# Optimization experiments

Measured on AMD Instinct MI355X. Metric: run time of the kernel, lower is better.

## Reference

```python
import jax, jax.numpy as jnp
import numpy as np

N_TOKENS = 65536
D_MODEL = 256
N_EXPERTS = 32
NEG_INF = -1e38


def setup_inputs() -> dict:
    key = jax.random.key(0)
    k_x, k_wg, k_wn, k_we, k_noise = jax.random.split(key, 5)
    x = jax.random.normal(k_x, (N_TOKENS, D_MODEL), dtype=jnp.float32)
    # gating and noise projections: Linear(d_model -> n_experts), no bias
    Wg = jax.random.normal(k_wg, (D_MODEL, N_EXPERTS), dtype=jnp.float32) * 0.02
    Wnoise = jax.random.normal(k_wn, (D_MODEL, N_EXPERTS), dtype=jnp.float32) * 0.02
    # experts: one Linear(d_model -> d_model) per expert
    We = jax.random.normal(k_we, (N_EXPERTS, D_MODEL, D_MODEL), dtype=jnp.float32) * 0.02
    be = jnp.zeros((N_EXPERTS, D_MODEL), dtype=jnp.float32)
    # torch.randn(nexperts): one shared noise vector broadcast over tokens
    noise_vec = jax.random.normal(k_noise, (N_EXPERTS,), dtype=jnp.float32)
    return {"x": x, "Wg": Wg, "Wnoise": Wnoise, "We": We, "be": be,
            "noise_vec": noise_vec, "top_k": 2}


def reference(x, Wg, Wnoise, We, be, noise_vec, top_k):
    # Eq. (4): H = x Wg + randn * softplus(x Wnoise)   -> [N, E]
    g = x @ Wg
    H = g + noise_vec[None, :] * jax.nn.softplus(x @ Wnoise)
    # Keep top_k largest per row (original masks the bottom E-k with -Inf)
    vals, idx = jax.lax.top_k(H, top_k)                      # [N, k]
    rows = jnp.arange(H.shape[0])[:, None]
    keep = jnp.full_like(H, NEG_INF).at[rows, idx].set(vals)  # [N, E]
    G = jax.nn.softmax(keep, axis=1)                          # [N, E], k nonzeros
    # Dense all-expert compute (as in the original): E_out [N, E, D]
    E_out = jnp.einsum('nd,edh->neh', x, We) + be[None, :, :]
    # Weighted sum over experts
    return jnp.einsum('ne,neh->nh', G, E_out)                 # [N, D]
```

## Files before the change

### kernel.cpp

```cpp
#include <hip/hip_runtime.h>

#define NT 65536
#define DM 256
#define NE 32

typedef __attribute__((ext_vector_type(8))) short v8bf;
typedef __attribute__((ext_vector_type(4))) float v4f;

#define C_RISKY 0
#define C_TC1 1
#define C_TC2 2
#define C_HIST1 8
#define C_HIST2 40
#define C_CUR1 72
#define C_CUR2 104

__device__ __forceinline__ unsigned short f2bf(float f) {
  union { float f; unsigned u; } v; v.f = f;
  unsigned r = v.u + 0x7FFFu + ((v.u >> 16) & 1u);
  return (unsigned short)(r >> 16);
}

#define GLOAD_LDS16(g, l)                                                     \
  __builtin_amdgcn_global_load_lds(                                           \
      (const __attribute__((address_space(1))) unsigned int*)(g),             \
      (__attribute__((address_space(3))) unsigned int*)(l), 16, 0, 0)

__global__ __launch_bounds__(256) void convert_kernel(const float* __restrict__ x,
                                                      unsigned short* __restrict__ xbf) {
  size_t i = (size_t)blockIdx.x * 256 + threadIdx.x;
  const float4* s = (const float4*)x + i * 2;
  float4 a = s[0], b = s[1];
  union { v8bf v; unsigned short u[8]; uint4 q; } p;
  p.u[0] = f2bf(a.x); p.u[1] = f2bf(a.y); p.u[2] = f2bf(a.z); p.u[3] = f2bf(a.w);
  p.u[4] = f2bf(b.x); p.u[5] = f2bf(b.y); p.u[6] = f2bf(b.z); p.u[7] = f2bf(b.w);
  *(uint4*)(xbf + i * 8) = p.q;
}

__global__ __launch_bounds__(256) void prep_w(const float* __restrict__ Wg,
                                              const float* __restrict__ Wn,
                                              float* __restrict__ wgn,
                                              unsigned short* __restrict__ wgnb) {
  int i = blockIdx.x * 256 + threadIdx.x;
  if (i < 256 * 64) {
    int k = i >> 6, c = i & 63;
    float v = (c < 32) ? Wg[k * 32 + c] : Wn[k * 32 + (c - 32)];
    wgn[i] = v;
    wgnb[c * 256 + k] = f2bf(v);
  }
}

__global__ __launch_bounds__(256) void prep_wet(const float* __restrict__ We,
                                                unsigned short* __restrict__ WeT) {
  __shared__ float t[32][33];
  int e = blockIdx.x;
  int d0 = (blockIdx.y >> 3) * 32, h0 = (blockIdx.y & 7) * 32;
  int tx = threadIdx.x & 31, ty = threadIdx.x >> 5;
  const float* src = We + ((size_t)e * 256 + d0) * 256 + h0;
#pragma unroll
  for (int r = 0; r < 4; ++r) t[ty + r * 8][tx] = src[(size_t)(ty + r * 8) * 256 + tx];
  __syncthreads();
  unsigned short* dst = WeT + ((size_t)e * 256 + h0) * 256 + d0;
#pragma unroll
  for (int r = 0; r < 4; ++r) dst[(size_t)(ty + r * 8) * 256 + tx] = f2bf(t[tx][ty + r * 8]);
}

__global__ __launch_bounds__(256) void gate_kernel(const float* __restrict__ x,
                                                   const unsigned short* __restrict__ xbf,
                                                   int use_xbf,
                                                   const unsigned short* __restrict__ wgnb,
                                                   const float* __restrict__ nvec,
                                                   int4* __restrict__ records,
                                                   int* __restrict__ risky,
                                                   int* __restrict__ ctrl) {
  __shared__ __align__(16) union {
    struct { short Al[128 * 64]; short Bl[64 * 64]; } t;
    float H[128 * 67];
  } sm;
  __shared__ float nvs[32];
  __shared__ int lh[64];
  int tid = threadIdx.x;
  if (tid < 64) lh[tid] = 0;
  if (tid < 32) nvs[tid] = nvec[tid];
  int t0 = blockIdx.x * 128;
  int lane = tid & 63, wid = tid >> 6;
  int wm = wid * 32;
  int lm = lane & 15, lk8 = (lane >> 4) * 8;
  int r0 = tid >> 3, kc = tid & 7;
  int kcs = kc ^ (r0 & 7);
  v4f acc[2][4];
  v4f zero = {0.f, 0.f, 0.f, 0.f};
#pragma unroll
  for (int mi = 0; mi < 2; ++mi)
#pragma unroll
    for (int ni = 0; ni < 4; ++ni) acc[mi][ni] = zero;
  for (int k0 = 0; k0 < 256; k0 += 64) {
    __syncthreads();
    if (use_xbf) {
#pragma unroll
      for (int j = 0; j < 4; ++j)
        GLOAD_LDS16(xbf + ((size_t)(t0 + r0 + 32 * j) * 256 + k0 + kcs * 8),
                    sm.t.Al + (size_t)(256 * j + (tid & 192)) * 8);
#pragma unroll
      for (int j = 0; j < 2; ++j)
        GLOAD_LDS16(wgnb + ((size_t)(r0 + 32 * j) * 256 + k0 + kcs * 8),
                    sm.t.Bl + (size_t)(256 * j + (tid & 192)) * 8);
    } else {
#pragma unroll
      for (int j = 0; j < 4; ++j) {
        const float4* s = (const float4*)(x + ((size_t)(t0 + r0 + 32 * j) * 256 + k0 + kcs * 8));
        float4 a = s[0], b = s[1];
        union { v8bf v; unsigned short u[8]; } p;
        p.u[0] = f2bf(a.x); p.u[1] = f2bf(a.y); p.u[2] = f2bf(a.z); p.u[3] = f2bf(a.w);
        p.u[4] = f2bf(b.x); p.u[5] = f2bf(b.y); p.u[6] = f2bf(b.z); p.u[7] = f2bf(b.w);
        *(v8bf*)(sm.t.Al + (size_t)(tid + 256 * j) * 8) = p.v;
      }
#pragma unroll
      for (int j = 0; j < 2; ++j) {
        uint4 w = *(const uint4*)(wgnb + ((size_t)(r0 + 32 * j) * 256 + k0 + kcs * 8));
        *(uint4*)(sm.t.Bl + (size_t)(tid + 256 * j) * 8) = w;
      }
    }
    __syncthreads();
#pragma unroll
    for (int ks = 0; ks < 64; ks += 32) {
      int c = (ks + lk8) >> 3;
      int cs = c ^ (lm & 7);
      v8bf af[2], bfr[4];
#pragma unroll
      for (int mi = 0; mi < 2; ++mi) {
        int r = wm + mi * 16 + lm;
        af[mi] = *(const v8bf*)(sm.t.Al + (size_t)(r * 8 + cs) * 8);
      }
#pragma unroll
      for (int ni = 0; ni < 4; ++ni) {
        int cr = ni * 16 + lm;
        bfr[ni] = *(const v8bf*)(sm.t.Bl + (size_t)(cr * 8 + cs) * 8);
      }
#pragma unroll
      for (int mi = 0; mi < 2; ++mi)
#pragma unroll
        for (int ni = 0; ni < 4; ++ni)
          acc[mi][ni] = __builtin_amdgcn_mfma_f32_16x16x32_bf16(af[mi], bfr[ni], acc[mi][ni], 0, 0, 0);
    }
  }
  __syncthreads();
  int cg = lane & 15, rg = lane >> 4;
#pragma unroll
  for (int mi = 0; mi < 2; ++mi)
#pragma unroll
    for (int r = 0; r < 4; ++r) {
      int row = wm + mi * 16 + rg * 4 + r;
#pragma unroll
      for (int ni = 0; ni < 4; ++ni) sm.H[row * 67 + ni * 16 + cg] = acc[mi][ni][r];
    }
  __syncthreads();
  if (tid < 128) {
    int t = t0 + tid;
    float v1 = -3e38f, v2 = -3e38f, v3 = -3e38f;
    int i1 = 0, i2 = 0;
#pragma unroll 4
    for (int e = 0; e < 32; ++e) {
      float g = sm.H[tid * 67 + e];
      float n = sm.H[tid * 67 + 32 + e];
      float sp = fmaxf(n, 0.f) + log1pf(expf(-fabsf(n)));
      float he = fmaf(nvs[e], sp, g);
      if (he > v1) { v3 = v2; v2 = v1; i2 = i1; v1 = he; i1 = e; }
      else if (he > v2) { v3 = v2; v2 = he; i2 = e; }
      else if (he > v3) v3 = he;
    }
    float w1v = 1.f / (1.f + expf(v2 - v1));
    float w2v = 1.f / (1.f + expf(v1 - v2));
    records[t] = make_int4(i1, i2, __float_as_int(w1v), __float_as_int(w2v));
    atomicAdd(&lh[i1], 1);
    atomicAdd(&lh[32 + i2], 1);
    if (v2 - v3 < 2e-2f) {
      int p = atomicAdd(&ctrl[C_RISKY], 1);
      risky[p] = t;
    }
  }
  __syncthreads();
  if (tid < 32) atomicAdd(&ctrl[C_HIST1 + tid], lh[tid]);
  else if (tid < 64) atomicAdd(&ctrl[C_HIST2 + (tid - 32)], lh[tid]);
}

__global__ __launch_bounds__(256) void fixup_kernel(const float* __restrict__ x,
                                                    const float* __restrict__ wgn,
                                                    const float* __restrict__ nvec,
                                                    int4* __restrict__ records,
                                                    const int* __restrict__ risky,
                                                    int* __restrict__ ctrl) {
  int cnt = ctrl[C_RISKY];
  int lane = threadIdx.x & 63, wid = threadIdx.x >> 6;
  for (int r = blockIdx.x * 4 + wid; r < cnt; r += gridDim.x * 4) {
    int t = __builtin_amdgcn_readfirstlane(risky[r]);
    const float* xr = x + (size_t)t * 256;
    double a0 = 0.0, a1 = 0.0, a2 = 0.0, a3 = 0.0;
    for (int k = 0; k < 256; k += 4) {
      float4 xv = *(const float4*)(xr + k);
      a0 = fma((double)xv.x, (double)wgn[(k + 0) * 64 + lane], a0);
      a1 = fma((double)xv.y, (double)wgn[(k + 1) * 64 + lane], a1);
      a2 = fma((double)xv.z, (double)wgn[(k + 2) * 64 + lane], a2);
      a3 = fma((double)xv.w, (double)wgn[(k + 3) * 64 + lane], a3);
    }
    double acc = (a0 + a1) + (a2 + a3);
    double sv = __shfl(acc, lane + 32);
    double H;
    if (lane < 32) {
      double sp = fmax(sv, 0.0) + log1p(exp(-fabs(sv)));
      H = acc + (double)nvec[lane] * sp;
    } else
      H = -1e300;
    double v = H; int idx = lane;
#pragma unroll
    for (int off = 32; off >= 1; off >>= 1) {
      double ov = __shfl_xor(v, off); int oi = __shfl_xor(idx, off);
      if (ov > v || (ov == v && oi < idx)) { v = ov; idx = oi; }
    }
    int i1 = idx; double v1 = v;
    v = (lane == i1) ? -1e300 : H; idx = lane;
#pragma unroll
    for (int off = 32; off >= 1; off >>= 1) {
      double ov = __shfl_xor(v, off); int oi = __shfl_xor(idx, off);
      if (ov > v || (ov == v && oi < idx)) { v = ov; idx = oi; }
    }
    int i2 = idx; double v2 = v;
    if (lane == 0) {
      float w1v = (float)(1.0 / (1.0 + exp(v2 - v1)));
      float w2v = (float)(1.0 / (1.0 + exp(v1 - v2)));
      int4 old = records[t];
      if (old.x != i1) { atomicSub(&ctrl[C_HIST1 + old.x], 1); atomicAdd(&ctrl[C_HIST1 + i1], 1); }
      if (old.y != i2) { atomicSub(&ctrl[C_HIST2 + old.y], 1); atomicAdd(&ctrl[C_HIST2 + i2], 1); }
      records[t] = make_int4(i1, i2, __float_as_int(w1v), __float_as_int(w2v));
    }
  }
}

__global__ __launch_bounds__(64) void scan_kernel(int* __restrict__ ctrl,
                                                  int4* __restrict__ table1,
                                                  int4* __restrict__ table2) {
  __shared__ int so1[32], so2[32], tp1[32], tp2[32];
  int tid = threadIdx.x;
  if (tid == 0) {
    int o = 0, tp = 0;
    for (int e = 0; e < 32; ++e) {
      so1[e] = o; tp1[e] = tp;
      int c = ctrl[C_HIST1 + e];
      o += c; tp += (c + 127) >> 7;
    }
    ctrl[C_TC1] = tp;
    o = 0; tp = 0;
    for (int e = 0; e < 32; ++e) {
      so2[e] = o; tp2[e] = tp;
      int c = ctrl[C_HIST2 + e];
      o += c; tp += (c + 127) >> 7;
    }
    ctrl[C_TC2] = tp;
  }
  __syncthreads();
  if (tid < 32) {
    int e = tid;
    ctrl[C_CUR1 + e] = so1[e];
    int c = ctrl[C_HIST1 + e];
    int nt = (c + 127) >> 7;
    for (int m = 0; m < nt; ++m)
      table1[tp1[e] + m] = make_int4(e, so1[e] + m * 128, min(128, c - m * 128), 0);
  } else if (tid < 64) {
    int e = tid - 32;
    ctrl[C_CUR2 + e] = so2[e];
    int c = ctrl[C_HIST2 + e];
    int nt = (c + 127) >> 7;
    for (int m = 0; m < nt; ++m)
      table2[tp2[e] + m] = make_int4(e, so2[e] + m * 128, min(128, c - m * 128), 0);
  }
}

__global__ __launch_bounds__(256) void scatter_kernel(const int4* __restrict__ records,
                                                      int* __restrict__ ctrl,
                                                      int* __restrict__ perm1, float* __restrict__ pw1,
                                                      int* __restrict__ perm2, float* __restrict__ pw2) {
  __shared__ int lh1[32], lh2[32], b1[32], b2[32];
  int tid = threadIdx.x;
  if (tid < 32) { lh1[tid] = 0; lh2[tid] = 0; }
  __syncthreads();
  int t = blockIdx.x * 256 + tid;
  int4 rec = records[t];
  int r1 = atomicAdd(&lh1[rec.x], 1);
  int r2 = atomicAdd(&lh2[rec.y], 1);
  __syncthreads();
  if (tid < 32) {
    b1[tid] = atomicAdd(&ctrl[C_CUR1 + tid], lh1[tid]);
    b2[tid] = atomicAdd(&ctrl[C_CUR2 + tid], lh2[tid]);
  }
  __syncthreads();
  int s1 = b1[rec.x] + r1; perm1[s1] = t; pw1[s1] = __int_as_float(rec.z);
  int s2 = b2[rec.y] + r2; perm2[s2] = t; pw2[s2] = __int_as_float(rec.w);
}

__global__ __launch_bounds__(256) void expert_kernel(const float* __restrict__ x,
                                                     const unsigned short* __restrict__ xbf,
                                                     int use_xbf,
                                                     const unsigned short* __restrict__ WeT,
                                                     const float* __restrict__ be,
                                                     const int* __restrict__ perm,
                                                     const float* __restrict__ pw,
                                                     const int4* __restrict__ table,
                                                     const int* __restrict__ tcp,
                                                     float* __restrict__ out,
                                                     int accumulate) {
  int nt = *tcp;
  if (blockIdx.x >= nt) return;
  int4 ent = table[blockIdx.x];
  int e = ent.x, sbase = ent.y, rows = ent.z;
  int n0 = blockIdx.y * 128;
  __shared__ __align__(16) short Al[128 * 64];
  __shared__ __align__(16) short Bl[128 * 64];
  int tid = threadIdx.x;
  int lane = tid & 63, wid = tid >> 6;
  int wm = (wid & 1) * 64, wn = (wid >> 1) * 64;
  int lm = lane & 15, lk8 = (lane >> 4) * 8;
  int r0 = tid >> 3, kc = tid & 7;
  int kcs = kc ^ (r0 & 7);
  int tok[4];
#pragma unroll
  for (int j = 0; j < 4; ++j) tok[j] = perm[sbase + min(r0 + 32 * j, rows - 1)];
  v4f acc[4][4];
  v4f zero = {0.f, 0.f, 0.f, 0.f};
#pragma unroll
  for (int mi = 0; mi < 4; ++mi)
#pragma unroll
    for (int ni = 0; ni < 4; ++ni) acc[mi][ni] = zero;
  for (int k0 = 0; k0 < 256; k0 += 64) {
    __syncthreads();
    if (use_xbf) {
#pragma unroll
      for (int j = 0; j < 4; ++j)
        GLOAD_LDS16(xbf + ((size_t)tok[j] * 256 + k0 + kcs * 8),
                    Al + (size_t)(256 * j + (tid & 192)) * 8);
#pragma unroll
      for (int j = 0; j < 4; ++j)
        GLOAD_LDS16(WeT + (((size_t)e * 256 + n0 + r0 + 32 * j) * 256 + k0 + kcs * 8),
                    Bl + (size_t)(256 * j + (tid & 192)) * 8);
    } else {
#pragma unroll
      for (int j = 0; j < 4; ++j) {
        const float4* s = (const float4*)(x + ((size_t)tok[j] * 256 + k0 + kcs * 8));
        float4 a = s[0], b = s[1];
        union { v8bf v; unsigned short u[8]; } p;
        p.u[0] = f2bf(a.x); p.u[1] = f2bf(a.y); p.u[2] = f2bf(a.z); p.u[3] = f2bf(a.w);
        p.u[4] = f2bf(b.x); p.u[5] = f2bf(b.y); p.u[6] = f2bf(b.z); p.u[7] = f2bf(b.w);
        *(v8bf*)(Al + (size_t)(tid + 256 * j) * 8) = p.v;
      }
#pragma unroll
      for (int j = 0; j < 4; ++j) {
        uint4 w = *(const uint4*)(WeT + (((size_t)e * 256 + n0 + r0 + 32 * j) * 256 + k0 + kcs * 8));
        *(uint4*)(Bl + (size_t)(tid + 256 * j) * 8) = w;
      }
    }
    __syncthreads();
#pragma unroll
    for (int ks = 0; ks < 64; ks += 32) {
      int c = (ks + lk8) >> 3;
      int cs = c ^ (lm & 7);
      v8bf af[4], bfr[4];
#pragma unroll
      for (int mi = 0; mi < 4; ++mi) {
        int r = wm + mi * 16 + lm;
        af[mi] = *(const v8bf*)(Al + (size_t)(r * 8 + cs) * 8);
      }
#pragma unroll
      for (int ni = 0; ni < 4; ++ni) {
        int cr = wn + ni * 16 + lm;
        bfr[ni] = *(const v8bf*)(Bl + (size_t)(cr * 8 + cs) * 8);
      }
#pragma unroll
      for (int mi = 0; mi < 4; ++mi)
#pragma unroll
        for (int ni = 0; ni < 4; ++ni)
          acc[mi][ni] = __builtin_amdgcn_mfma_f32_16x16x32_bf16(af[mi], bfr[ni], acc[mi][ni], 0, 0, 0);
    }
  }
  int cg = lane & 15, rg = lane >> 4;
#pragma unroll
  for (int mi = 0; mi < 4; ++mi) {
#pragma unroll
    for (int r = 0; r < 4; ++r) {
      int srow = wm + mi * 16 + rg * 4 + r;
      if (srow < rows) {
        int slot = sbase + srow;
        int tokr = perm[slot];
        float w = pw[slot];
        size_t ob = (size_t)tokr * 256;
#pragma unroll
        for (int ni = 0; ni < 4; ++ni) {
          int c = n0 + wn + ni * 16 + cg;
          float v = acc[mi][ni][r] * w + w * be[e * 256 + c];
          if (accumulate) out[ob + c] += v;
          else out[ob + c] = v;
        }
      }
    }
  }
}

extern "C" void kernel_launch(void* const* d_in, const int* in_sizes, int n_in,
                              void* d_out, int out_size, void* d_ws, size_t ws_size,
                              hipStream_t stream) {
  const float* x = (const float*)d_in[0];
  const float* Wg = (const float*)d_in[1];
  const float* Wn = (const float*)d_in[2];
  const float* We = (const float*)d_in[3];
  const float* be = (const float*)d_in[4];
  const float* nvec = (const float*)d_in[5];
  float* out = (float*)d_out;
  char* ws = (char*)d_ws;
  size_t off = 0;
  auto alloc = [&](size_t bytes) -> void* {
    void* p = ws + off;
    off = (off + bytes + 255) & ~(size_t)255;
    return p;
  };
  int* ctrl = (int*)alloc(4096);
  int4* records = (int4*)alloc((size_t)NT * 16);
  int* risky = (int*)alloc((size_t)NT * 4);
  int* perm1 = (int*)alloc((size_t)NT * 4);
  float* pw1 = (float*)alloc((size_t)NT * 4);
  int* perm2 = (int*)alloc((size_t)NT * 4);
  float* pw2 = (float*)alloc((size_t)NT * 4);
  int4* table1 = (int4*)alloc(1024 * 16);
  int4* table2 = (int4*)alloc(1024 * 16);
  float* wgn = (float*)alloc(256 * 64 * 4);
  unsigned short* wgnb = (unsigned short*)alloc(64 * 256 * 2);
  unsigned short* WeT = (unsigned short*)alloc((size_t)NE * 256 * 256 * 2);
  unsigned short* xbf = nullptr;
  int use_xbf = 0;
  if (off + (size_t)NT * 256 * 2 <= ws_size) {
    xbf = (unsigned short*)alloc((size_t)NT * 256 * 2);
    use_xbf = 1;
  }

  hipMemsetAsync(ctrl, 0, 4096, stream);
  prep_w<<<64, 256, 0, stream>>>(Wg, Wn, wgn, wgnb);
  prep_wet<<<dim3(32, 64), 256, 0, stream>>>(We, WeT);
  if (use_xbf) convert_kernel<<<NT * DM / 8 / 256, 256, 0, stream>>>(x, xbf);
  gate_kernel<<<NT / 128, 256, 0, stream>>>(x, xbf, use_xbf, wgnb, nvec, records, risky, ctrl);
  fixup_kernel<<<256, 256, 0, stream>>>(x, wgn, nvec, records, risky, ctrl);
  scan_kernel<<<1, 64, 0, stream>>>(ctrl, table1, table2);
  scatter_kernel<<<NT / 256, 256, 0, stream>>>(records, ctrl, perm1, pw1, perm2, pw2);
  expert_kernel<<<dim3(544, 2), 256, 0, stream>>>(x, xbf, use_xbf, WeT, be, perm1, pw1, table1,
                                                  ctrl + C_TC1, out, 0);
  expert_kernel<<<dim3(544, 2), 256, 0, stream>>>(x, xbf, use_xbf, WeT, be, perm2, pw2, table2,
                                                  ctrl + C_TC2, out, 1);
}
```

Before: 406.6 us.

## Stage second-expert outputs in bf16 buffer and widen expert K-tile to 128

The second-choice expert pass now writes its weighted outputs as bf16 into a slot-indexed buffer instead of doing a read-modify-write on the fp32 output. The first-choice pass reads that buffer through a token-to-slot map and writes the final sum once. This removes the fp32 read of out during accumulation. The expert GEMM also loads 128-wide K tiles, which halves the number of K iterations and barriers but doubles LDS use and may lower occupancy. Rounding the partial result to bf16 adds some precision loss.

```diff
diff --git a/kernel.cpp b/kernel.cpp
--- a/kernel.cpp
+++ b/kernel.cpp
@@ -19,6 +19,9 @@
   union { float f; unsigned u; } v; v.f = f;
   unsigned r = v.u + 0x7FFFu + ((v.u >> 16) & 1u);
   return (unsigned short)(r >> 16);
+}
+__device__ __forceinline__ float bf2f(unsigned short b) {
+  union { unsigned u; float f; } v; v.u = ((unsigned)b) << 16; return v.f;
 }
 
 #define GLOAD_LDS16(g, l)                                                     \
@@ -128,15 +131,11 @@
       int cs = c ^ (lm & 7);
       v8bf af[2], bfr[4];
 #pragma unroll
-      for (int mi = 0; mi < 2; ++mi) {
-        int r = wm + mi * 16 + lm;
-        af[mi] = *(const v8bf*)(sm.t.Al + (size_t)(r * 8 + cs) * 8);
-      }
-#pragma unroll
-      for (int ni = 0; ni < 4; ++ni) {
-        int cr = ni * 16 + lm;
-        bfr[ni] = *(const v8bf*)(sm.t.Bl + (size_t)(cr * 8 + cs) * 8);
-      }
+      for (int mi = 0; mi < 2; ++mi)
+        af[mi] = *(const v8bf*)(sm.t.Al + (size_t)((wm + mi * 16 + lm) * 8 + cs) * 8);
+#pragma unroll
+      for (int ni = 0; ni < 4; ++ni)
+        bfr[ni] = *(const v8bf*)(sm.t.Bl + (size_t)((ni * 16 + lm) * 8 + cs) * 8);
 #pragma unroll
       for (int mi = 0; mi < 2; ++mi)
 #pragma unroll
@@ -278,7 +277,8 @@
 __global__ __launch_bounds__(256) void scatter_kernel(const int4* __restrict__ records,
                                                       int* __restrict__ ctrl,
                                                       int* __restrict__ perm1, float* __restrict__ pw1,
-                                                      int* __restrict__ perm2, float* __restrict__ pw2) {
+                                                      int* __restrict__ perm2, float* __restrict__ pw2,
+                                                      int* __restrict__ tpos2) {
   __shared__ int lh1[32], lh2[32], b1[32], b2[32];
   int tid = threadIdx.x;
   if (tid < 32) { lh1[tid] = 0; lh2[tid] = 0; }
@@ -295,6 +295,7 @@
   __syncthreads();
   int s1 = b1[rec.x] + r1; perm1[s1] = t; pw1[s1] = __int_as_float(rec.z);
   int s2 = b2[rec.y] + r2; perm2[s2] = t; pw2[s2] = __int_as_float(rec.w);
+  tpos2[t] = s2;
 }
 
 __global__ __launch_bounds__(256) void expert_kernel(const float* __restrict__ x,
@@ -304,75 +305,81 @@
                                                      const float* __restrict__ be,
                                                      const int* __restrict__ perm,
                                                      const float* __restrict__ pw,
+                                                     const int* __restrict__ tpos2,
+                                                     unsigned short* __restrict__ y1,
                                                      const int4* __restrict__ table,
                                                      const int* __restrict__ tcp,
                                                      float* __restrict__ out,
-                                                     int accumulate) {
+                                                     int mode) {
   int nt = *tcp;
   if (blockIdx.x >= nt) return;
   int4 ent = table[blockIdx.x];
   int e = ent.x, sbase = ent.y, rows = ent.z;
   int n0 = blockIdx.y * 128;
-  __shared__ __align__(16) short Al[128 * 64];
-  __shared__ __align__(16) short Bl[128 * 64];
+  __shared__ __align__(16) short Al[128 * 128];
+  __shared__ __align__(16) short Bl[128 * 128];
   int tid = threadIdx.x;
   int lane = tid & 63, wid = tid >> 6;
   int wm = (wid & 1) * 64, wn = (wid >> 1) * 64;
   int lm = lane & 15, lk8 = (lane >> 4) * 8;
-  int r0 = tid >> 3, kc = tid & 7;
-  int kcs = kc ^ (r0 & 7);
-  int tok[4];
-#pragma unroll
-  for (int j = 0; j < 4; ++j) tok[j] = perm[sbase + min(r0 + 32 * j, rows - 1)];
+  int hb = lane >> 4;
+  int cl = lane & 15;
+  int tokA[8];
+#pragma unroll
+  for (int i = 0; i < 8; ++i)
+    tokA[i] = perm[sbase + min(wid * 32 + 4 * i + hb, rows - 1)];
   v4f acc[4][4];
   v4f zero = {0.f, 0.f, 0.f, 0.f};
 #pragma unroll
   for (int mi = 0; mi < 4; ++mi)
 #pragma unroll
     for (int ni = 0; ni < 4; ++ni) acc[mi][ni] = zero;
-  for (int k0 = 0; k0 < 256; k0 += 64) {
+  for (int k0 = 0; k0 < 256; k0 += 128) {
     __syncthreads();
     if (use_xbf) {
 #pragma unroll
-      for (int j = 0; j < 4; ++j)
-        GLOAD_LDS16(xbf + ((size_t)tok[j] * 256 + k0 + kcs * 8),
-                    Al + (size_t)(256 * j + (tid & 192)) * 8);
-#pragma unroll
-      for (int j = 0; j < 4; ++j)
-        GLOAD_LDS16(WeT + (((size_t)e * 256 + n0 + r0 + 32 * j) * 256 + k0 + kcs * 8),
-                    Bl + (size_t)(256 * j + (tid & 192)) * 8);
+      for (int i = 0; i < 8; ++i) {
+        int row = wid * 32 + 4 * i + hb;
+        int csrc = cl ^ (row & 7);
+        GLOAD_LDS16(xbf + ((size_t)tokA[i] * 256 + k0 + csrc * 8),
+                    Al + (size_t)(wid * 32 + 4 * i) * 128);
+      }
+#pragma unroll
+      for (int i = 0; i < 8; ++i) {
+        int row = wid * 32 + 4 * i + hb;
+        int csrc = cl ^ (row & 7);
+        GLOAD_LDS16(WeT + (((size_t)e * 256 + n0 + row) * 256 + k0 + csrc * 8),
+                    Bl + (size_t)(wid * 32 + 4 * i) * 128);
+      }
     } else {
 #pragma unroll
-      for (int j = 0; j < 4; ++j) {
-        const float4* s = (const float4*)(x + ((size_t)tok[j] * 256 + k0 + kcs * 8));
+      for (int j = 0; j < 8; ++j) {
+        int idx = tid + 256 * j;
+        int row = idx >> 4, cslot = idx & 15;
+        int csrc = cslot ^ (row & 7);
+        int tokr = perm[sbase + min(row, rows - 1)];
+        const float4* s = (const float4*)(x + ((size_t)tokr * 256 + k0 + csrc * 8));
         float4 a = s[0], b = s[1];
         union { v8bf v; unsigned short u[8]; } p;
         p.u[0] = f2bf(a.x); p.u[1] = f2bf(a.y); p.u[2] = f2bf(a.z); p.u[3] = f2bf(a.w);
         p.u[4] = f2bf(b.x); p.u[5] = f2bf(b.y); p.u[6] = f2bf(b.z); p.u[7] = f2bf(b.w);
-        *(v8bf*)(Al + (size_t)(tid + 256 * j) * 8) = p.v;
-      }
-#pragma unroll
-      for (int j = 0; j < 4; ++j) {
-        uint4 w = *(const uint4*)(WeT + (((size_t)e * 256 + n0 + r0 + 32 * j) * 256 + k0 + kcs * 8));
-        *(uint4*)(Bl + (size_t)(tid + 256 * j) * 8) = w;
+        *(v8bf*)(Al + (size_t)(row * 16 + cslot) * 8) = p.v;
+        uint4 w = *(const uint4*)(WeT + (((size_t)e * 256 + n0 + row) * 256 + k0 + csrc * 8));
+        *(uint4*)(Bl + (size_t)(row * 16 + cslot) * 8) = w;
       }
     }
     __syncthreads();
 #pragma unroll
-    for (int ks = 0; ks < 64; ks += 32) {
+    for (int ks = 0; ks < 128; ks += 32) {
       int c = (ks + lk8) >> 3;
       int cs = c ^ (lm & 7);
       v8bf af[4], bfr[4];
 #pragma unroll
-      for (int mi = 0; mi < 4; ++mi) {
-        int r = wm + mi * 16 + lm;
-        af[mi] = *(const v8bf*)(Al + (size_t)(r * 8 + cs) * 8);
-      }
-#pragma unroll
-      for (int ni = 0; ni < 4; ++ni) {
-        int cr = wn + ni * 16 + lm;
-        bfr[ni] = *(const v8bf*)(Bl + (size_t)(cr * 8 + cs) * 8);
-      }
+      for (int mi = 0; mi < 4; ++mi)
+        af[mi] = *(const v8bf*)(Al + (size_t)((wm + mi * 16 + lm) * 16 + cs) * 8);
+#pragma unroll
+      for (int ni = 0; ni < 4; ++ni)
+        bfr[ni] = *(const v8bf*)(Bl + (size_t)((wn + ni * 16 + lm) * 16 + cs) * 8);
 #pragma unroll
       for (int mi = 0; mi < 4; ++mi)
 #pragma unroll
@@ -388,15 +395,36 @@
       int srow = wm + mi * 16 + rg * 4 + r;
       if (srow < rows) {
         int slot = sbase + srow;
-        int tokr = perm[slot];
         float w = pw[slot];
-        size_t ob = (size_t)tokr * 256;
-#pragma unroll
-        for (int ni = 0; ni < 4; ++ni) {
-          int c = n0 + wn + ni * 16 + cg;
-          float v = acc[mi][ni][r] * w + w * be[e * 256 + c];
-          if (accumulate) out[ob + c] += v;
-          else out[ob + c] = v;
+        if (mode == 0) {
+          unsigned short* yrow = y1 + (size_t)slot * 256 + n0 + wn;
+#pragma unroll
+          for (int ni = 0; ni < 4; ++ni) {
+            int c = ni * 16 + cg;
+            float v = acc[mi][ni][r] * w + w * be[e * 256 + n0 + wn + c];
+            yrow[c] = f2bf(v);
+          }
+        } else if (mode == 1) {
+          int tokr = perm[slot];
+          int s2 = tpos2[tokr];
+          const unsigned short* yr = y1 + (size_t)s2 * 256 + n0 + wn;
+          float* orow = out + (size_t)tokr * 256 + n0 + wn;
+#pragma unroll
+          for (int ni = 0; ni < 4; ++ni) {
+            int c = ni * 16 + cg;
+            float v = acc[mi][ni][r] * w + w * be[e * 256 + n0 + wn + c];
+            orow[c] = v + bf2f(yr[c]);
+          }
+        } else {
+          int tokr = perm[slot];
+          float* orow = out + (size_t)tokr * 256 + n0 + wn;
+#pragma unroll
+          for (int ni = 0; ni < 4; ++ni) {
+            int c = ni * 16 + cg;
+            float v = acc[mi][ni][r] * w + w * be[e * 256 + n0 + wn + c];
+            if (mode == 3) orow[c] += v;
+            else orow[c] = v;
+          }
         }
       }
     }
@@ -427,6 +455,7 @@
   float* pw1 = (float*)alloc((size_t)NT * 4);
   int* perm2 = (int*)alloc((size_t)NT * 4);
   float* pw2 = (float*)alloc((size_t)NT * 4);
+  int* tpos2 = (int*)alloc((size_t)NT * 4);
   int4* table1 = (int4*)alloc(1024 * 16);
   int4* table2 = (int4*)alloc(1024 * 16);
   float* wgn = (float*)alloc(256 * 64 * 4);
@@ -438,6 +467,12 @@
     xbf = (unsigned short*)alloc((size_t)NT * 256 * 2);
     use_xbf = 1;
   }
+  unsigned short* y1 = nullptr;
+  int use_y1 = 0;
+  if (off + (size_t)NT * 256 * 2 <= ws_size) {
+    y1 = (unsigned short*)alloc((size_t)NT * 256 * 2);
+    use_y1 = 1;
+  }
 
   hipMemsetAsync(ctrl, 0, 4096, stream);
   prep_w<<<64, 256, 0, stream>>>(Wg, Wn, wgn, wgnb);
@@ -446,9 +481,16 @@
   gate_kernel<<<NT / 128, 256, 0, stream>>>(x, xbf, use_xbf, wgnb, nvec, records, risky, ctrl);
   fixup_kernel<<<256, 256, 0, stream>>>(x, wgn, nvec, records, risky, ctrl);
   scan_kernel<<<1, 64, 0, stream>>>(ctrl, table1, table2);
-  scatter_kernel<<<NT / 256, 256, 0, stream>>>(records, ctrl, perm1, pw1, perm2, pw2);
-  expert_kernel<<<dim3(544, 2), 256, 0, stream>>>(x, xbf, use_xbf, WeT, be, perm1, pw1, table1,
-                                                  ctrl + C_TC1, out, 0);
-  expert_kernel<<<dim3(544, 2), 256, 0, stream>>>(x, xbf, use_xbf, WeT, be, perm2, pw2, table2,
-                                                  ctrl + C_TC2, out, 1);
-}
+  scatter_kernel<<<NT / 256, 256, 0, stream>>>(records, ctrl, perm1, pw1, perm2, pw2, tpos2);
+  if (use_y1) {
+    expert_kernel<<<dim3(544, 2), 256, 0, stream>>>(x, xbf, use_xbf, WeT, be, perm2, pw2,
+                                                    tpos2, y1, table2, ctrl + C_TC2, out, 0);
+    expert_kernel<<<dim3(544, 2), 256, 0, stream>>>(x, xbf, use_xbf, WeT, be, perm1, pw1,
+                                                    tpos2, y1, table1, ctrl + C_TC1, out, 1);
+  } else {
+    expert_kernel<<<dim3(544, 2), 256, 0, stream>>>(x, xbf, use_xbf, WeT, be, perm1, pw1,
+                                                    tpos2, y1, table1, ctrl + C_TC1, out, 2);
+    expert_kernel<<<dim3(544, 2), 256, 0, stream>>>(x, xbf, use_xbf, WeT, be, perm2, pw2,
+                                                    tpos2, y1, table2, ctrl + C_TC2, out, 3);
+  }
+}
```

Measured after the change: 368.7 us. 9.3% less time.

## Restructure expert GEMM: 64-row tiles, double-buffered loads, bf16 intermediate combine

Applied to the files above, without the earlier changes.

Expert tiles shrink from 128 to 64 rows, and each block now covers the full 256 output columns instead of half. K-slices of 32 are double-buffered through LDS using async global-to-LDS loads with explicit waitcnt and barriers. The second expert result is no longer written by read-modify-write on the fp32 output. The first pass writes bf16 partial results to a slot-indexed buffer, and the second pass reads them back through a token-to-slot map and writes each output row once with coalesced float4 stores staged in LDS. The fp32-x fallback path is removed, which makes the bf16 x copy mandatory and adds a second NT×256 bf16 workspace; storing the intermediate in bf16 slightly reduces precision.

```diff
diff --git a/kernel.cpp b/kernel.cpp
--- a/kernel.cpp
+++ b/kernel.cpp
@@ -15,10 +15,18 @@
 #define C_CUR1 72
 #define C_CUR2 104
 
+#define W_VM(n) (0xF70 | (n))
+
 __device__ __forceinline__ unsigned short f2bf(float f) {
   union { float f; unsigned u; } v; v.f = f;
   unsigned r = v.u + 0x7FFFu + ((v.u >> 16) & 1u);
   return (unsigned short)(r >> 16);
+}
+__device__ __forceinline__ float bflo(unsigned u) {
+  union { unsigned x; float f; } v; v.x = u << 16; return v.f;
+}
+__device__ __forceinline__ float bfhi(unsigned u) {
+  union { unsigned x; float f; } v; v.x = u & 0xFFFF0000u; return v.f;
 }
 
 #define GLOAD_LDS16(g, l)                                                     \
@@ -65,9 +73,7 @@
   for (int r = 0; r < 4; ++r) dst[(size_t)(ty + r * 8) * 256 + tx] = f2bf(t[tx][ty + r * 8]);
 }
 
-__global__ __launch_bounds__(256) void gate_kernel(const float* __restrict__ x,
-                                                   const unsigned short* __restrict__ xbf,
-                                                   int use_xbf,
+__global__ __launch_bounds__(256) void gate_kernel(const unsigned short* __restrict__ xbf,
                                                    const unsigned short* __restrict__ wgnb,
                                                    const float* __restrict__ nvec,
                                                    int4* __restrict__ records,
@@ -96,31 +102,14 @@
     for (int ni = 0; ni < 4; ++ni) acc[mi][ni] = zero;
   for (int k0 = 0; k0 < 256; k0 += 64) {
     __syncthreads();
-    if (use_xbf) {
-#pragma unroll
-      for (int j = 0; j < 4; ++j)
-        GLOAD_LDS16(xbf + ((size_t)(t0 + r0 + 32 * j) * 256 + k0 + kcs * 8),
-                    sm.t.Al + (size_t)(256 * j + (tid & 192)) * 8);
-#pragma unroll
-      for (int j = 0; j < 2; ++j)
-        GLOAD_LDS16(wgnb + ((size_t)(r0 + 32 * j) * 256 + k0 + kcs * 8),
-                    sm.t.Bl + (size_t)(256 * j + (tid & 192)) * 8);
-    } else {
-#pragma unroll
-      for (int j = 0; j < 4; ++j) {
-        const float4* s = (const float4*)(x + ((size_t)(t0 + r0 + 32 * j) * 256 + k0 + kcs * 8));
-        float4 a = s[0], b = s[1];
-        union { v8bf v; unsigned short u[8]; } p;
-        p.u[0] = f2bf(a.x); p.u[1] = f2bf(a.y); p.u[2] = f2bf(a.z); p.u[3] = f2bf(a.w);
-        p.u[4] = f2bf(b.x); p.u[5] = f2bf(b.y); p.u[6] = f2bf(b.z); p.u[7] = f2bf(b.w);
-        *(v8bf*)(sm.t.Al + (size_t)(tid + 256 * j) * 8) = p.v;
-      }
-#pragma unroll
-      for (int j = 0; j < 2; ++j) {
-        uint4 w = *(const uint4*)(wgnb + ((size_t)(r0 + 32 * j) * 256 + k0 + kcs * 8));
-        *(uint4*)(sm.t.Bl + (size_t)(tid + 256 * j) * 8) = w;
-      }
-    }
+#pragma unroll
+    for (int j = 0; j < 4; ++j)
+      GLOAD_LDS16(xbf + ((size_t)(t0 + r0 + 32 * j) * 256 + k0 + kcs * 8),
+                  sm.t.Al + (size_t)(256 * j + (tid & 192)) * 8);
+#pragma unroll
+    for (int j = 0; j < 2; ++j)
+      GLOAD_LDS16(wgnb + ((size_t)(r0 + 32 * j) * 256 + k0 + kcs * 8),
+                  sm.t.Bl + (size_t)(256 * j + (tid & 192)) * 8);
     __syncthreads();
 #pragma unroll
     for (int ks = 0; ks < 64; ks += 32) {
@@ -128,15 +117,11 @@
       int cs = c ^ (lm & 7);
       v8bf af[2], bfr[4];
 #pragma unroll
-      for (int mi = 0; mi < 2; ++mi) {
-        int r = wm + mi * 16 + lm;
-        af[mi] = *(const v8bf*)(sm.t.Al + (size_t)(r * 8 + cs) * 8);
-      }
-#pragma unroll
-      for (int ni = 0; ni < 4; ++ni) {
-        int cr = ni * 16 + lm;
-        bfr[ni] = *(const v8bf*)(sm.t.Bl + (size_t)(cr * 8 + cs) * 8);
-      }
+      for (int mi = 0; mi < 2; ++mi)
+        af[mi] = *(const v8bf*)(sm.t.Al + (size_t)((wm + mi * 16 + lm) * 8 + cs) * 8);
+#pragma unroll
+      for (int ni = 0; ni < 4; ++ni)
+        bfr[ni] = *(const v8bf*)(sm.t.Bl + (size_t)((ni * 16 + lm) * 8 + cs) * 8);
 #pragma unroll
       for (int mi = 0; mi < 2; ++mi)
 #pragma unroll
@@ -246,14 +231,14 @@
     for (int e = 0; e < 32; ++e) {
       so1[e] = o; tp1[e] = tp;
       int c = ctrl[C_HIST1 + e];
-      o += c; tp += (c + 127) >> 7;
+      o += c; tp += (c + 63) >> 6;
     }
     ctrl[C_TC1] = tp;
     o = 0; tp = 0;
     for (int e = 0; e < 32; ++e) {
       so2[e] = o; tp2[e] = tp;
       int c = ctrl[C_HIST2 + e];
-      o += c; tp += (c + 127) >> 7;
+      o += c; tp += (c + 63) >> 6;
     }
     ctrl[C_TC2] = tp;
   }
@@ -262,23 +247,24 @@
     int e = tid;
     ctrl[C_CUR1 + e] = so1[e];
     int c = ctrl[C_HIST1 + e];
-    int nt = (c + 127) >> 7;
+    int nt = (c + 63) >> 6;
     for (int m = 0; m < nt; ++m)
-      table1[tp1[e] + m] = make_int4(e, so1[e] + m * 128, min(128, c - m * 128), 0);
+      table1[tp1[e] + m] = make_int4(e, so1[e] + m * 64, min(64, c - m * 64), 0);
   } else if (tid < 64) {
     int e = tid - 32;
     ctrl[C_CUR2 + e] = so2[e];
     int c = ctrl[C_HIST2 + e];
-    int nt = (c + 127) >> 7;
+    int nt = (c + 63) >> 6;
     for (int m = 0; m < nt; ++m)
-      table2[tp2[e] + m] = make_int4(e, so2[e] + m * 128, min(128, c - m * 128), 0);
+      table2[tp2[e] + m] = make_int4(e, so2[e] + m * 64, min(64, c - m * 64), 0);
   }
 }
 
 __global__ __launch_bounds__(256) void scatter_kernel(const int4* __restrict__ records,
                                                       int* __restrict__ ctrl,
                                                       int* __restrict__ perm1, float* __restrict__ pw1,
-                                                      int* __restrict__ perm2, float* __restrict__ pw2) {
+                                                      int* __restrict__ perm2, float* __restrict__ pw2,
+                                                      int* __restrict__ tpos2) {
   __shared__ int lh1[32], lh2[32], b1[32], b2[32];
   int tid = threadIdx.x;
   if (tid < 32) { lh1[tid] = 0; lh2[tid] = 0; }
@@ -295,111 +281,147 @@
   __syncthreads();
   int s1 = b1[rec.x] + r1; perm1[s1] = t; pw1[s1] = __int_as_float(rec.z);
   int s2 = b2[rec.y] + r2; perm2[s2] = t; pw2[s2] = __int_as_float(rec.w);
-}
-
-__global__ __launch_bounds__(256) void expert_kernel(const float* __restrict__ x,
-                                                     const unsigned short* __restrict__ xbf,
-                                                     int use_xbf,
+  tpos2[t] = s2;
+}
+
+__global__ __launch_bounds__(256) void expert_kernel(const unsigned short* __restrict__ xbf,
                                                      const unsigned short* __restrict__ WeT,
                                                      const float* __restrict__ be,
                                                      const int* __restrict__ perm,
                                                      const float* __restrict__ pw,
+                                                     const int* __restrict__ tpos2,
+                                                     unsigned short* __restrict__ y1,
                                                      const int4* __restrict__ table,
                                                      const int* __restrict__ tcp,
                                                      float* __restrict__ out,
-                                                     int accumulate) {
+                                                     int mode) {
   int nt = *tcp;
   if (blockIdx.x >= nt) return;
   int4 ent = table[blockIdx.x];
   int e = ent.x, sbase = ent.y, rows = ent.z;
-  int n0 = blockIdx.y * 128;
-  __shared__ __align__(16) short Al[128 * 64];
-  __shared__ __align__(16) short Bl[128 * 64];
-  int tid = threadIdx.x;
-  int lane = tid & 63, wid = tid >> 6;
-  int wm = (wid & 1) * 64, wn = (wid >> 1) * 64;
-  int lm = lane & 15, lk8 = (lane >> 4) * 8;
-  int r0 = tid >> 3, kc = tid & 7;
-  int kcs = kc ^ (r0 & 7);
-  int tok[4];
-#pragma unroll
-  for (int j = 0; j < 4; ++j) tok[j] = perm[sbase + min(r0 + 32 * j, rows - 1)];
+  __shared__ __align__(16) union {
+    struct { short A[2 * 4 * 64 * 8]; short B[2 * 4 * 256 * 8]; } st;
+    float epi[32 * 8 * 36];
+  } sm;
+  __shared__ int toksh[64];
+  __shared__ int s2sh[64];
+  __shared__ float pwsh[64];
+  __shared__ float bel[256];
+  int tid = threadIdx.x, lane = tid & 63, w = tid >> 6;
+  if (tid < 64) {
+    int slot = sbase + min(tid, rows - 1);
+    int tk = perm[slot];
+    toksh[tid] = tk;
+    pwsh[tid] = pw[slot];
+    s2sh[tid] = (mode == 1) ? tpos2[tk] : 0;
+  }
+  bel[tid] = be[e * 256 + tid];
+  __syncthreads();
+  const unsigned short* tokptr = xbf + (size_t)toksh[lane] * 256;
+  const unsigned short* wptr = WeT + ((size_t)e * 256 + w * 64 + lane) * 256;
+
   v4f acc[4][4];
   v4f zero = {0.f, 0.f, 0.f, 0.f};
 #pragma unroll
   for (int mi = 0; mi < 4; ++mi)
 #pragma unroll
     for (int ni = 0; ni < 4; ++ni) acc[mi][ni] = zero;
-  for (int k0 = 0; k0 < 256; k0 += 64) {
-    __syncthreads();
-    if (use_xbf) {
-#pragma unroll
-      for (int j = 0; j < 4; ++j)
-        GLOAD_LDS16(xbf + ((size_t)tok[j] * 256 + k0 + kcs * 8),
-                    Al + (size_t)(256 * j + (tid & 192)) * 8);
-#pragma unroll
-      for (int j = 0; j < 4; ++j)
-        GLOAD_LDS16(WeT + (((size_t)e * 256 + n0 + r0 + 32 * j) * 256 + k0 + kcs * 8),
-                    Bl + (size_t)(256 * j + (tid & 192)) * 8);
-    } else {
-#pragma unroll
-      for (int j = 0; j < 4; ++j) {
-        const float4* s = (const float4*)(x + ((size_t)tok[j] * 256 + k0 + kcs * 8));
-        float4 a = s[0], b = s[1];
-        union { v8bf v; unsigned short u[8]; } p;
-        p.u[0] = f2bf(a.x); p.u[1] = f2bf(a.y); p.u[2] = f2bf(a.z); p.u[3] = f2bf(a.w);
-        p.u[4] = f2bf(b.x); p.u[5] = f2bf(b.y); p.u[6] = f2bf(b.z); p.u[7] = f2bf(b.w);
-        *(v8bf*)(Al + (size_t)(tid + 256 * j) * 8) = p.v;
-      }
-#pragma unroll
-      for (int j = 0; j < 4; ++j) {
-        uint4 w = *(const uint4*)(WeT + (((size_t)e * 256 + n0 + r0 + 32 * j) * 256 + k0 + kcs * 8));
-        *(uint4*)(Bl + (size_t)(tid + 256 * j) * 8) = w;
-      }
-    }
-    __syncthreads();
-#pragma unroll
-    for (int ks = 0; ks < 64; ks += 32) {
-      int c = (ks + lk8) >> 3;
-      int cs = c ^ (lm & 7);
-      v8bf af[4], bfr[4];
-#pragma unroll
-      for (int mi = 0; mi < 4; ++mi) {
-        int r = wm + mi * 16 + lm;
-        af[mi] = *(const v8bf*)(Al + (size_t)(r * 8 + cs) * 8);
-      }
-#pragma unroll
-      for (int ni = 0; ni < 4; ++ni) {
-        int cr = wn + ni * 16 + lm;
-        bfr[ni] = *(const v8bf*)(Bl + (size_t)(cr * 8 + cs) * 8);
-      }
-#pragma unroll
-      for (int mi = 0; mi < 4; ++mi)
-#pragma unroll
-        for (int ni = 0; ni < 4; ++ni)
-          acc[mi][ni] = __builtin_amdgcn_mfma_f32_16x16x32_bf16(af[mi], bfr[ni], acc[mi][ni], 0, 0, 0);
-    }
-  }
+
+  auto stage = [&](int buf, int k0) {
+    GLOAD_LDS16(tokptr + k0 + w * 8, sm.st.A + (size_t)(buf * 4 + w) * 64 * 8);
+#pragma unroll
+    for (int b = 0; b < 4; ++b)
+      GLOAD_LDS16(wptr + k0 + b * 8,
+                  sm.st.B + ((size_t)(buf * 4 + b) * 256 + w * 64) * 8);
+  };
+  auto compute = [&](int buf) {
+    int q = lane >> 4, lm = lane & 15;
+    v8bf a[4], bfr[4];
+#pragma unroll
+    for (int mi = 0; mi < 4; ++mi)
+      a[mi] = *(const v8bf*)(sm.st.A + ((size_t)(buf * 4 + q) * 64 + mi * 16 + lm) * 8);
+#pragma unroll
+    for (int ni = 0; ni < 4; ++ni)
+      bfr[ni] = *(const v8bf*)(sm.st.B + ((size_t)(buf * 4 + q) * 256 + w * 64 + ni * 16 + lm) * 8);
+#pragma unroll
+    for (int mi = 0; mi < 4; ++mi)
+#pragma unroll
+      for (int ni = 0; ni < 4; ++ni)
+        acc[mi][ni] = __builtin_amdgcn_mfma_f32_16x16x32_bf16(a[mi], bfr[ni], acc[mi][ni], 0, 0, 0);
+  };
+
+  stage(0, 0);
+#pragma unroll
+  for (int s = 0; s < 8; ++s) {
+    if (s < 7) stage((s + 1) & 1, (s + 1) * 32);
+    if (s < 7) __builtin_amdgcn_s_waitcnt(W_VM(5));
+    else __builtin_amdgcn_s_waitcnt(W_VM(0));
+    __builtin_amdgcn_s_barrier();
+    compute(s & 1);
+    __builtin_amdgcn_s_barrier();
+  }
+
   int cg = lane & 15, rg = lane >> 4;
 #pragma unroll
-  for (int mi = 0; mi < 4; ++mi) {
-#pragma unroll
-    for (int r = 0; r < 4; ++r) {
-      int srow = wm + mi * 16 + rg * 4 + r;
-      if (srow < rows) {
-        int slot = sbase + srow;
-        int tokr = perm[slot];
-        float w = pw[slot];
-        size_t ob = (size_t)tokr * 256;
+  for (int half = 0; half < 2; ++half) {
+#pragma unroll
+    for (int m2 = 0; m2 < 2; ++m2) {
+      int mi = half * 2 + m2;
+#pragma unroll
+      for (int rr = 0; rr < 4; ++rr) {
+        int row = mi * 16 + rg * 4 + rr;
+        int lrow = row - half * 32;
+        float wv = pwsh[row];
 #pragma unroll
         for (int ni = 0; ni < 4; ++ni) {
-          int c = n0 + wn + ni * 16 + cg;
-          float v = acc[mi][ni][r] * w + w * be[e * 256 + c];
-          if (accumulate) out[ob + c] += v;
-          else out[ob + c] = v;
+          int seg = w * 2 + (ni >> 1);
+          int c = (ni & 1) * 16 + cg;
+          float v = (acc[mi][ni][rr] + bel[w * 64 + ni * 16 + cg]) * wv;
+          sm.epi[(lrow * 8 + seg) * 36 + c] = v;
         }
       }
     }
+    __syncthreads();
+    {
+      int lrow = tid >> 3, seg = tid & 7;
+      int grow = half * 32 + lrow;
+      if (grow < rows) {
+        int slot = sbase + grow;
+        int tk = toksh[grow];
+        const float* ep = &sm.epi[(lrow * 8 + seg) * 36];
+        if (mode == 0) {
+          uint4* yp = (uint4*)(y1 + (size_t)slot * 256 + seg * 32);
+#pragma unroll
+          for (int i = 0; i < 4; ++i) {
+            float4 p0 = *(const float4*)(ep + i * 8);
+            float4 p1 = *(const float4*)(ep + i * 8 + 4);
+            uint4 q;
+            q.x = ((unsigned)f2bf(p0.y) << 16) | f2bf(p0.x);
+            q.y = ((unsigned)f2bf(p0.w) << 16) | f2bf(p0.z);
+            q.z = ((unsigned)f2bf(p1.y) << 16) | f2bf(p1.x);
+            q.w = ((unsigned)f2bf(p1.w) << 16) | f2bf(p1.z);
+            yp[i] = q;
+          }
+        } else {
+          int s2 = s2sh[grow];
+          const uint4* yp = (const uint4*)(y1 + (size_t)s2 * 256 + seg * 32);
+          float4* op = (float4*)(out + (size_t)tk * 256 + seg * 32);
+#pragma unroll
+          for (int i = 0; i < 4; ++i) {
+            uint4 yq = yp[i];
+            float4 p0 = *(const float4*)(ep + i * 8);
+            float4 p1 = *(const float4*)(ep + i * 8 + 4);
+            p0.x += bflo(yq.x); p0.y += bfhi(yq.x);
+            p0.z += bflo(yq.y); p0.w += bfhi(yq.y);
+            p1.x += bflo(yq.z); p1.y += bfhi(yq.z);
+            p1.z += bflo(yq.w); p1.w += bfhi(yq.w);
+            op[i * 2] = p0;
+            op[i * 2 + 1] = p1;
+          }
+        }
+      }
+    }
+    __syncthreads();
   }
 }
 
@@ -427,28 +449,25 @@
   float* pw1 = (float*)alloc((size_t)NT * 4);
   int* perm2 = (int*)alloc((size_t)NT * 4);
   float* pw2 = (float*)alloc((size_t)NT * 4);
-  int4* table1 = (int4*)alloc(1024 * 16);
-  int4* table2 = (int4*)alloc(1024 * 16);
+  int* tpos2 = (int*)alloc((size_t)NT * 4);
+  int4* table1 = (int4*)alloc(2048 * 16);
+  int4* table2 = (int4*)alloc(2048 * 16);
   float* wgn = (float*)alloc(256 * 64 * 4);
   unsigned short* wgnb = (unsigned short*)alloc(64 * 256 * 2);
+  unsigned short* xbf = (unsigned short*)alloc((size_t)NT * 256 * 2);
+  unsigned short* y1 = (unsigned short*)alloc((size_t)NT * 256 * 2);
   unsigned short* WeT = (unsigned short*)alloc((size_t)NE * 256 * 256 * 2);
-  unsigned short* xbf = nullptr;
-  int use_xbf = 0;
-  if (off + (size_t)NT * 256 * 2 <= ws_size) {
-    xbf = (unsigned short*)alloc((size_t)NT * 256 * 2);
-    use_xbf = 1;
-  }
 
   hipMemsetAsync(ctrl, 0, 4096, stream);
   prep_w<<<64, 256, 0, stream>>>(Wg, Wn, wgn, wgnb);
   prep_wet<<<dim3(32, 64), 256, 0, stream>>>(We, WeT);
-  if (use_xbf) convert_kernel<<<NT * DM / 8 / 256, 256, 0, stream>>>(x, xbf);
-  gate_kernel<<<NT / 128, 256, 0, stream>>>(x, xbf, use_xbf, wgnb, nvec, records, risky, ctrl);
+  convert_kernel<<<NT * DM / 8 / 256, 256, 0, stream>>>(x, xbf);
+  gate_kernel<<<NT / 128, 256, 0, stream>>>(xbf, wgnb, nvec, records, risky, ctrl);
   fixup_kernel<<<256, 256, 0, stream>>>(x, wgn, nvec, records, risky, ctrl);
   scan_kernel<<<1, 64, 0, stream>>>(ctrl, table1, table2);
-  scatter_kernel<<<NT / 256, 256, 0, stream>>>(records, ctrl, perm1, pw1, perm2, pw2);
-  expert_kernel<<<dim3(544, 2), 256, 0, stream>>>(x, xbf, use_xbf, WeT, be, perm1, pw1, table1,
-                                                  ctrl + C_TC1, out, 0);
-  expert_kernel<<<dim3(544, 2), 256, 0, stream>>>(x, xbf, use_xbf, WeT, be, perm2, pw2, table2,
-                                                  ctrl + C_TC2, out, 1);
-}
+  scatter_kernel<<<NT / 256, 256, 0, stream>>>(records, ctrl, perm1, pw1, perm2, pw2, tpos2);
+  expert_kernel<<<1088, 256, 0, stream>>>(xbf, WeT, be, perm2, pw2, tpos2, y1,
+                                          table2, ctrl + C_TC2, out, 0);
+  expert_kernel<<<1088, 256, 0, stream>>>(xbf, WeT, be, perm1, pw1, tpos2, y1,
+                                          table1, ctrl + C_TC1, out, 1);
+}
```

Measured after the change: 375.9 us. 7.5% less time.
